# Kernel optimization log

Measured on AMD Instinct MI355X. Metric: run time of the kernel, lower is better.

Reference implementation:

```python
import jax, jax.numpy as jnp
import numpy as np

IN_DIM = 512
HID = 1024
E = 16
TOPK = 2


def setup_inputs() -> dict:
    key = jax.random.key(0)
    ks = jax.random.split(key, 8)
    s = 0.02
    x = jax.random.normal(ks[0], (4, 2048, IN_DIM), dtype=jnp.float32)
    Wr = jax.random.normal(ks[1], (IN_DIM, E), dtype=jnp.float32) * s
    br = jnp.zeros((E,), dtype=jnp.float32)
    W1 = jax.random.normal(ks[2], (E, IN_DIM, HID), dtype=jnp.float32) * s
    b1 = jnp.zeros((E, HID), dtype=jnp.float32)
    W2 = jax.random.normal(ks[3], (E, HID, IN_DIM), dtype=jnp.float32) * s
    b2 = jnp.zeros((E, IN_DIM), dtype=jnp.float32)
    return {"x": x, "Wr": Wr, "br": br, "W1": W1, "b1": b1, "W2": W2, "b2": b2}


def reference(x, Wr, br, W1, b1, W2, b2):
    token_shape = x.shape[:-1]
    xf = x.reshape(-1, x.shape[-1])            # [T, D]
    T = xf.shape[0]

    # router (temperature = 1.0)
    logits = xf @ Wr + br                       # [T, E]
    probs = jax.nn.softmax(logits, axis=-1)
    topk_w, topk_idx = jax.lax.top_k(probs, TOPK)           # [T, K]
    topk_w = topk_w / jnp.maximum(topk_w.sum(-1, keepdims=True), 1e-9)

    # combine weights: [T, E], zero where not routed
    combine = jnp.zeros((T, E), dtype=xf.dtype).at[
        jnp.arange(T)[:, None], topk_idx].add(topk_w)

    # per-expert MLP (exact GELU, as torch nn.GELU default), weighted combine
    y = jnp.zeros_like(xf)
    for e in range(E):
        h = jax.nn.gelu(xf @ W1[e] + b1[e], approximate=False)  # [T, H]
        o = h @ W2[e] + b2[e]                                   # [T, D]
        y = y + combine[:, e:e + 1] * o

    # residual (in_dim == out_dim)
    y = xf + y
    return y.reshape(*token_shape, IN_DIM)
```

## Files before the change

### kernel.cpp

```cpp
#include <hip/hip_runtime.h>
#include <hip/hip_bf16.h>
#include <math.h>

#define IN_DIM 512
#define HID    1024
#define NE     16
#define T_TOK  8192
#define NPAIR  (T_TOK*2)

typedef __attribute__((ext_vector_type(8))) short bf16x8;
typedef __attribute__((ext_vector_type(8))) unsigned short ushort8;
typedef __attribute__((ext_vector_type(4))) float f32x4;

__device__ __forceinline__ unsigned short f2b(float f){
  unsigned u = __float_as_uint(f);
  u += 0x7FFF + ((u >> 16) & 1);
  return (unsigned short)(u >> 16);
}
__device__ __forceinline__ float b2f(unsigned short u){
  return __uint_as_float(((unsigned)u) << 16);
}

__device__ __forceinline__ void barrier_lds_only(){
  asm volatile("s_waitcnt lgkmcnt(0)" ::: "memory");
  __builtin_amdgcn_s_barrier();
}

__global__ __launch_bounds__(256) void fused_head(
    const float* __restrict__ x, const float* __restrict__ Wr, const float* __restrict__ br,
    unsigned short* __restrict__ xb, int* __restrict__ eid, float* __restrict__ pw,
    const float* __restrict__ W1, unsigned short* __restrict__ O1,
    const float* __restrict__ W2, unsigned short* __restrict__ O2)
{
  __shared__ float tile[64][65];
  const int b = blockIdx.x;
  const int tid = threadIdx.x;

  if (b < 2048){
    int wid = tid >> 6, lane = tid & 63;
    int t = b*4 + wid;
    const float4* xr4 = (const float4*)(x + (size_t)t*IN_DIM);
    ushort4*      xb4 = (ushort4*)(xb + (size_t)t*IN_DIM);

    float acc[NE];
    #pragma unroll
    for (int i=0;i<NE;i++) acc[i]=0.f;

    #pragma unroll
    for (int j=0;j<2;j++){
      int f = j*64 + lane;
      float4 v = xr4[f];
      ushort4 o; o.x=f2b(v.x); o.y=f2b(v.y); o.z=f2b(v.z); o.w=f2b(v.w);
      xb4[f] = o;
      const float4* wr4 = (const float4*)(Wr + (size_t)(f*4)*NE);
      const float* vv = (const float*)&v;
      #pragma unroll
      for (int rr=0; rr<4; rr++){
        float xv = vv[rr];
        #pragma unroll
        for (int q=0;q<4;q++){
          float4 w = wr4[rr*4+q];
          acc[q*4+0] += xv*w.x; acc[q*4+1] += xv*w.y;
          acc[q*4+2] += xv*w.z; acc[q*4+3] += xv*w.w;
        }
      }
    }
    #pragma unroll
    for (int off=32; off>=1; off>>=1){
      #pragma unroll
      for (int i=0;i<NE;i++) acc[i] += __shfl_xor(acc[i], off, 64);
    }
    if (lane==0){
      #pragma unroll
      for (int i=0;i<NE;i++) acc[i] += br[i];
      int e0=0; float l0=acc[0];
      #pragma unroll
      for (int i=1;i<NE;i++) if (acc[i] > l0){ l0=acc[i]; e0=i; }
      int e1=-1; float l1=-3.0e38f;
      #pragma unroll
      for (int i=0;i<NE;i++) if (i!=e0 && acc[i] > l1){ l1=acc[i]; e1=i; }
      float w0 = 1.f/(1.f + __expf(l1 - l0));
      float w1 = 1.f - w0;
      pw[t*2+0] = w0; pw[t*2+1] = w1;
      eid[t*2+0] = e0; eid[t*2+1] = e1;
    }
    return;
  }

  const float* src; unsigned short* dst; int M, N, m0, n0;
  if (b < 4096){
    int b1 = b - 2048; M = IN_DIM; N = HID;
    int e = b1 >> 7, r = b1 & 127;
    n0 = (r & 15)*64; m0 = (r >> 4)*64;
    src = W1 + (size_t)e*M*N; dst = O1 + (size_t)e*M*N;
  } else {
    int b2 = b - 4096; M = HID; N = IN_DIM;
    int e = b2 >> 7, r = b2 & 127;
    n0 = (r & 7)*64; m0 = (r >> 3)*64;
    src = W2 + (size_t)e*M*N; dst = O2 + (size_t)e*M*N;
  }
  const int lr = tid >> 4, lc = (tid & 15)*4;
  #pragma unroll
  for (int i=0;i<4;i++)
    *(float4*)&tile[lr + i*16][lc] = *(const float4*)&src[(size_t)(m0 + lr + i*16)*N + n0 + lc];
  __syncthreads();
  const int nr = tid >> 3, mc = (tid & 7)*8;
  #pragma unroll
  for (int p=0;p<2;p++){
    int n = nr + p*32;
    ushort8 o;
    #pragma unroll
    for (int j=0;j<8;j++) o[j] = f2b(tile[mc+j][n]);
    *(ushort8*)&dst[(size_t)(n0 + n)*M + m0 + mc] = o;
  }
}

__global__ __launch_bounds__(1024) void bucket_kernel(const int* __restrict__ eid,
                                                      int* __restrict__ cnt,
                                                      int* __restrict__ bucket){
  int e = blockIdx.x;
  __shared__ int lbase;
  if (threadIdx.x == 0) lbase = 0;
  __syncthreads();
  int lane = threadIdx.x & 63, wid = threadIdx.x >> 6;
  int* be = bucket + e*T_TOK;
  for (int c = wid*64; c < NPAIR; c += 1024){
    int p = c + lane;
    bool ok = (eid[p] == e);
    unsigned long long m = __ballot(ok);
    int rank = __popcll(m & ((1ull << lane) - 1ull));
    int count = __popcll(m);
    int base = 0;
    if (lane == 0) base = atomicAdd(&lbase, count);
    base = __shfl(base, 0, 64);
    if (ok) be[base + rank] = p;
  }
  __syncthreads();
  if (threadIdx.x == 0) cnt[e] = lbase;
}

template<int KDIM, int NDIM, bool FIRST>
__global__ __launch_bounds__(256) void moe_gemm(
    const unsigned short* __restrict__ A,
    const unsigned short* __restrict__ Bm,
    const float* __restrict__ bias,
    const int* __restrict__ cnt,
    const int* __restrict__ bucket,
    const float* __restrict__ pw,
    unsigned short* __restrict__ hb,
    unsigned short* __restrict__ opb)
{
  constexpr int NS  = KDIM / 32;
  constexpr int NBT = NDIM / 128;

  int ntiles = 0;
  #pragma unroll
  for (int j=0;j<NE;j++) ntiles += ((cnt[j]+63)>>6)*NBT;

  __shared__ unsigned short As[2*64*32];
  __shared__ unsigned short Bs[2*128*32];

  int tid = threadIdx.x;
  int lane = tid & 63, wid = tid >> 6;
  int wm = (wid>>1)*32, wn = (wid&1)*64;
  int lr0 = tid >> 2;
  int c   = tid & 3;
  int sc  = (c ^ ((lr0 >> 1) & 3)) * 8;
  int wA  = lr0*32 + sc;
  int fr = lane & 15, fb = lane >> 4;
  int pf8 = (fb ^ ((fr >> 1) & 3)) * 8;
  int fq = (lane>>4)*4;

  const int t0 = (blockIdx.x & 7)*(gridDim.x >> 3) + (blockIdx.x >> 3);
  for (int t = t0; t < ntiles; t += gridDim.x){
    int e=0, tloc=0, ebase=0, ce=0, itl=1;
    {
      int cum=0, crow=0;
      #pragma unroll
      for (int j=0;j<NE;j++){
        int cj = cnt[j];
        int it = (cj+63)>>6;
        int tj = it * NBT;
        bool in = (t >= cum) & (t < cum+tj);
        if (in){ e=j; tloc=t-cum; ebase=crow; ce=cj; itl=it; }
        cum += tj; crow += cj;
      }
    }
    int i0 = (tloc % itl) * 64;
    int n0 = (tloc / itl) * 128;

    const int* buck = bucket + e*T_TOK;
    int posA = i0 + lr0;
    int arow;
    if (FIRST){
      int pair = (posA < ce) ? buck[posA] : buck[i0];
      arow = pair >> 1;
    } else {
      arow = ebase + posA;
      if (arow > NPAIR-1) arow = NPAIR-1;
    }
    const unsigned short* Ag = A + (size_t)arow*KDIM + c*8;
    const unsigned short* Bg = Bm + (size_t)e*NDIM*KDIM + (size_t)(n0 + lr0)*KDIM + c*8;

    f32x4 acc[2][4];
    #pragma unroll
    for (int a=0;a<2;a++)
      #pragma unroll
      for (int b=0;b<4;b++)
        #pragma unroll
        for (int j=0;j<4;j++) acc[a][b][j] = 0.f;

    float4 ar, br0, br1;
    ar  = *(const float4*)(Ag);
    br0 = *(const float4*)(Bg);
    br1 = *(const float4*)(Bg + (size_t)64*KDIM);
    *(float4*)(As + wA) = ar;
    *(float4*)(Bs + wA) = br0;
    *(float4*)(Bs + wA + 64*32) = br1;
    ar  = *(const float4*)(Ag + 32);
    br0 = *(const float4*)(Bg + 32);
    br1 = *(const float4*)(Bg + (size_t)64*KDIM + 32);
    barrier_lds_only();

    #pragma unroll 2
    for (int k = 0; k < NS; k++){
      const int cur = k & 1, nxt = cur ^ 1;
      float4 na, nb0, nb1;
      bool ld = (k + 2 < NS);
      if (ld){
        na  = *(const float4*)(Ag + (k+2)*32);
        nb0 = *(const float4*)(Bg + (k+2)*32);
        nb1 = *(const float4*)(Bg + (size_t)64*KDIM + (k+2)*32);
      }
      if (k + 1 < NS){
        *(float4*)(As + nxt*2048 + wA) = ar;
        *(float4*)(Bs + nxt*4096 + wA) = br0;
        *(float4*)(Bs + nxt*4096 + wA + 64*32) = br1;
      }
      if (ld){ ar = na; br0 = nb0; br1 = nb1; }

      const unsigned short* Ac = As + cur*2048;
      const unsigned short* Bc = Bs + cur*4096;
      bf16x8 af[2], bfr[4];
      #pragma unroll
      for (int s=0;s<2;s++) af[s]  = *(const bf16x8*)(Ac + (wm + s*16 + fr)*32 + pf8);
      #pragma unroll
      for (int u=0;u<4;u++) bfr[u] = *(const bf16x8*)(Bc + (wn + u*16 + fr)*32 + pf8);
      #pragma unroll
      for (int s=0;s<2;s++)
        #pragma unroll
        for (int u=0;u<4;u++)
          acc[s][u] = __builtin_amdgcn_mfma_f32_16x16x32_bf16(af[s], bfr[u], acc[s][u], 0,0,0);
      barrier_lds_only();
    }

    #pragma unroll
    for (int s=0;s<2;s++){
      #pragma unroll
      for (int i=0;i<4;i++){
        int row = wm + s*16 + fq + i;
        int pos = i0 + row;
        if (pos >= ce) continue;
        #pragma unroll
        for (int u=0;u<4;u++){
          int n = n0 + wn + u*16 + fr;
          float v = acc[s][u][i] + bias[e*NDIM + n];
          if (FIRST){
            float z2 = v*(1.5957691216057308f + 0.0713548162726009f*v*v);
            float g  = __fdividef(v, 1.f + __expf(-z2));
            hb[(size_t)(ebase + pos)*NDIM + n] = f2b(g);
          } else {
            int pair = buck[pos];
            opb[(size_t)pair*NDIM + n] = f2b(pw[pair]*v);
          }
        }
      }
    }
  }
}

__global__ __launch_bounds__(256) void combine_kernel(const float* __restrict__ x,
                                                      const unsigned short* __restrict__ opb,
                                                      float* __restrict__ out){
  int i = blockIdx.x*256 + threadIdx.x;
  int t  = i >> 7;
  int c4 = i & 127;
  float4 v = ((const float4*)x)[i];
  ushort4 a = ((const ushort4*)opb)[(size_t)(2*t)*128 + c4];
  ushort4 b = ((const ushort4*)opb)[(size_t)(2*t+1)*128 + c4];
  v.x += b2f(a.x) + b2f(b.x);
  v.y += b2f(a.y) + b2f(b.y);
  v.z += b2f(a.z) + b2f(b.z);
  v.w += b2f(a.w) + b2f(b.w);
  ((float4*)out)[i] = v;
}

extern "C" void kernel_launch(void* const* d_in, const int* in_sizes, int n_in,
                              void* d_out, int out_size, void* d_ws, size_t ws_size,
                              hipStream_t stream)
{
  const float* x  = (const float*)d_in[0];
  const float* Wr = (const float*)d_in[1];
  const float* br = (const float*)d_in[2];
  const float* W1 = (const float*)d_in[3];
  const float* b1 = (const float*)d_in[4];
  const float* W2 = (const float*)d_in[5];
  const float* b2 = (const float*)d_in[6];
  float* out = (float*)d_out;
  char* ws = (char*)d_ws;

  int*            cnt    = (int*)(ws + 0);
  int*            bucket = (int*)(ws + 1024);
  float*          pw     = (float*)(ws + 525312);
  unsigned short* xb     = (unsigned short*)(ws + 590848);
  unsigned short* w1t    = (unsigned short*)(ws + 8979456);
  unsigned short* w2t    = (unsigned short*)(ws + 25756672);
  unsigned short* hb     = (unsigned short*)(ws + 42533888);
  int*            eid    = (int*)(ws + 42533888);
  unsigned short* opb    = w1t;

  fused_head<<<6144, 256, 0, stream>>>(x, Wr, br, xb, eid, pw, W1, w1t, W2, w2t);
  bucket_kernel<<<NE, 1024, 0, stream>>>(eid, cnt, bucket);
  moe_gemm<IN_DIM, HID, true ><<<1024, 256, 0, stream>>>(
      xb, w1t, b1, cnt, bucket, pw, hb, opb);
  moe_gemm<HID, IN_DIM, false><<<1024, 256, 0, stream>>>(
      hb, w2t, b2, cnt, bucket, pw, hb, opb);
  combine_kernel<<<(T_TOK*IN_DIM/4)/256, 256, 0, stream>>>(x, opb, out);
}
```

Before: 250.0 us.

## Restructure router into 64 blocks of 128 tokens with LDS-staged x

The router part of the fused head kernel now has 64 blocks, each handling 128 tokens, instead of 2048 blocks of one token per wavefront. It stages x chunks in swizzled shared memory and has one thread per token accumulate all 16 logits, which removes the 64-lane shuffle reduction and the repeated Wr loads per token. The trade-off is much less parallelism for the router work: only 128 threads per block compute, with a sequential loop over 8 chunks. This relies on overlapping that work with the weight-transpose blocks launched in the same grid.

Result: slower. 272.2 us (+8.9%).

```diff
diff --git a/kernel.cpp b/kernel.cpp
--- a/kernel.cpp
+++ b/kernel.cpp
@@ -7,6 +7,7 @@
 #define NE     16
 #define T_TOK  8192
 #define NPAIR  (T_TOK*2)
+#define NRB    64
 
 typedef __attribute__((ext_vector_type(8))) short bf16x8;
 typedef __attribute__((ext_vector_type(8))) unsigned short ushort8;
@@ -32,47 +33,49 @@
     const float* __restrict__ W1, unsigned short* __restrict__ O1,
     const float* __restrict__ W2, unsigned short* __restrict__ O2)
 {
-  __shared__ float tile[64][65];
+  __shared__ __align__(16) char smraw[32768];
   const int b = blockIdx.x;
-  const int tid = threadIdx.x;
-
-  if (b < 2048){
-    int wid = tid >> 6, lane = tid & 63;
-    int t = b*4 + wid;
-    const float4* xr4 = (const float4*)(x + (size_t)t*IN_DIM);
-    ushort4*      xb4 = (ushort4*)(xb + (size_t)t*IN_DIM);
-
+  const int t = threadIdx.x;
+
+  if (b < NRB){
+    float (*xs)[64] = (float(*)[64])smraw;
+    const int T0 = b*128;
+    const int tq = t & 15, ts = t >> 4;
     float acc[NE];
     #pragma unroll
-    for (int i=0;i<NE;i++) acc[i]=0.f;
-
-    #pragma unroll
-    for (int j=0;j<2;j++){
-      int f = j*64 + lane;
-      float4 v = xr4[f];
-      ushort4 o; o.x=f2b(v.x); o.y=f2b(v.y); o.z=f2b(v.z); o.w=f2b(v.w);
-      xb4[f] = o;
-      const float4* wr4 = (const float4*)(Wr + (size_t)(f*4)*NE);
-      const float* vv = (const float*)&v;
-      #pragma unroll
-      for (int rr=0; rr<4; rr++){
-        float xv = vv[rr];
+    for (int e=0;e<NE;e++) acc[e] = 0.f;
+    const bool comp = (t < 128);
+
+    #pragma unroll 1
+    for (int c = 0; c < 8; ++c){
+      #pragma unroll
+      for (int s = 0; s < 8; ++s){
+        int tok = s*16 + ts;
+        const float4 v = *(const float4*)&x[(size_t)(T0+tok)*IN_DIM + c*64 + tq*4];
+        ushort4 o; o.x=f2b(v.x); o.y=f2b(v.y); o.z=f2b(v.z); o.w=f2b(v.w);
+        *(ushort4*)&xb[(size_t)(T0+tok)*IN_DIM + c*64 + tq*4] = o;
+        *(float4*)&xs[tok][(tq ^ (tok & 15))*4] = v;
+      }
+      __syncthreads();
+      if (comp){
         #pragma unroll
-        for (int q=0;q<4;q++){
-          float4 w = wr4[rr*4+q];
-          acc[q*4+0] += xv*w.x; acc[q*4+1] += xv*w.y;
-          acc[q*4+2] += xv*w.z; acc[q*4+3] += xv*w.w;
+        for (int cc = 0; cc < 16; ++cc){
+          const float4 xv = *(const float4*)&xs[t][(cc ^ (t & 15))*4];
+          const float* wr = &Wr[(size_t)(c*64 + cc*4)*NE];
+          #pragma unroll
+          for (int j=0;j<4;j++){
+            const float xvj = ((const float*)&xv)[j];
+            #pragma unroll
+            for (int e=0;e<NE;e++) acc[e] += xvj * wr[j*NE + e];
+          }
         }
       }
-    }
-    #pragma unroll
-    for (int off=32; off>=1; off>>=1){
-      #pragma unroll
-      for (int i=0;i<NE;i++) acc[i] += __shfl_xor(acc[i], off, 64);
-    }
-    if (lane==0){
-      #pragma unroll
-      for (int i=0;i<NE;i++) acc[i] += br[i];
+      __syncthreads();
+    }
+
+    if (comp){
+      #pragma unroll
+      for (int e=0;e<NE;e++) acc[e] += br[e];
       int e0=0; float l0=acc[0];
       #pragma unroll
       for (int i=1;i<NE;i++) if (acc[i] > l0){ l0=acc[i]; e0=i; }
@@ -81,30 +84,33 @@
       for (int i=0;i<NE;i++) if (i!=e0 && acc[i] > l1){ l1=acc[i]; e1=i; }
       float w0 = 1.f/(1.f + __expf(l1 - l0));
       float w1 = 1.f - w0;
-      pw[t*2+0] = w0; pw[t*2+1] = w1;
-      eid[t*2+0] = e0; eid[t*2+1] = e1;
+      int tok = T0 + t;
+      pw[tok*2+0] = w0; pw[tok*2+1] = w1;
+      eid[tok*2+0] = e0; eid[tok*2+1] = e1;
     }
     return;
   }
 
+  float (*tile)[65] = (float(*)[65])smraw;
   const float* src; unsigned short* dst; int M, N, m0, n0;
-  if (b < 4096){
-    int b1 = b - 2048; M = IN_DIM; N = HID;
-    int e = b1 >> 7, r = b1 & 127;
+  const int bb = b - NRB;
+  if (bb < 2048){
+    M = IN_DIM; N = HID;
+    int e = bb >> 7, r = bb & 127;
     n0 = (r & 15)*64; m0 = (r >> 4)*64;
     src = W1 + (size_t)e*M*N; dst = O1 + (size_t)e*M*N;
   } else {
-    int b2 = b - 4096; M = HID; N = IN_DIM;
+    int b2 = bb - 2048; M = HID; N = IN_DIM;
     int e = b2 >> 7, r = b2 & 127;
     n0 = (r & 7)*64; m0 = (r >> 3)*64;
     src = W2 + (size_t)e*M*N; dst = O2 + (size_t)e*M*N;
   }
-  const int lr = tid >> 4, lc = (tid & 15)*4;
+  const int lr = t >> 4, lc = (t & 15)*4;
   #pragma unroll
   for (int i=0;i<4;i++)
     *(float4*)&tile[lr + i*16][lc] = *(const float4*)&src[(size_t)(m0 + lr + i*16)*N + n0 + lc];
   __syncthreads();
-  const int nr = tid >> 3, mc = (tid & 7)*8;
+  const int nr = t >> 3, mc = (t & 7)*8;
   #pragma unroll
   for (int p=0;p<2;p++){
     int n = nr + p*32;
@@ -206,9 +212,9 @@
     #pragma unroll
     for (int a=0;a<2;a++)
       #pragma unroll
-      for (int b=0;b<4;b++)
+      for (int b2=0;b2<4;b2++)
         #pragma unroll
-        for (int j=0;j<4;j++) acc[a][b][j] = 0.f;
+        for (int j=0;j<4;j++) acc[a][b2][j] = 0.f;
 
     float4 ar, br0, br1;
     ar  = *(const float4*)(Ag);
@@ -319,7 +325,7 @@
   int*            eid    = (int*)(ws + 42533888);
   unsigned short* opb    = w1t;
 
-  fused_head<<<6144, 256, 0, stream>>>(x, Wr, br, xb, eid, pw, W1, w1t, W2, w2t);
+  fused_head<<<NRB + 4096, 256, 0, stream>>>(x, Wr, br, xb, eid, pw, W1, w1t, W2, w2t);
   bucket_kernel<<<NE, 1024, 0, stream>>>(eid, cnt, bucket);
   moe_gemm<IN_DIM, HID, true ><<<1024, 256, 0, stream>>>(
       xb, w1t, b1, cnt, bucket, pw, hb, opb);
```

## Fuse expert bucketing into router via global atomics, drop bucket kernel

Applied to the files above, without the earlier changes.

The router lanes now reserve slots in per-expert buckets with global atomicAdd on counters cleared by a memset, which removes the separate bucket_kernel launch and the eid intermediate. The first expert GEMM's grid also grows from 1024 to 2048 blocks. Bucket order becomes nondeterministic, and contended atomics on 16 counters from 8192 tokens may serialize. There is also an extra memset launch.

New measurement: 401.5 us. 1.61x slower.

```diff
diff --git a/kernel.cpp b/kernel.cpp
--- a/kernel.cpp
+++ b/kernel.cpp
@@ -28,7 +28,8 @@
 
 __global__ __launch_bounds__(256) void fused_head(
     const float* __restrict__ x, const float* __restrict__ Wr, const float* __restrict__ br,
-    unsigned short* __restrict__ xb, int* __restrict__ eid, float* __restrict__ pw,
+    unsigned short* __restrict__ xb, int* __restrict__ cnt, int* __restrict__ bucket,
+    float* __restrict__ pw,
     const float* __restrict__ W1, unsigned short* __restrict__ O1,
     const float* __restrict__ W2, unsigned short* __restrict__ O2)
 {
@@ -82,19 +83,23 @@
       float w0 = 1.f/(1.f + __expf(l1 - l0));
       float w1 = 1.f - w0;
       pw[t*2+0] = w0; pw[t*2+1] = w1;
-      eid[t*2+0] = e0; eid[t*2+1] = e1;
+      int s0 = atomicAdd(&cnt[e0], 1);
+      bucket[e0*T_TOK + s0] = t*2+0;
+      int s1 = atomicAdd(&cnt[e1], 1);
+      bucket[e1*T_TOK + s1] = t*2+1;
     }
     return;
   }
 
   const float* src; unsigned short* dst; int M, N, m0, n0;
-  if (b < 4096){
-    int b1 = b - 2048; M = IN_DIM; N = HID;
-    int e = b1 >> 7, r = b1 & 127;
+  const int bb = b - 2048;
+  if (bb < 2048){
+    M = IN_DIM; N = HID;
+    int e = bb >> 7, r = bb & 127;
     n0 = (r & 15)*64; m0 = (r >> 4)*64;
     src = W1 + (size_t)e*M*N; dst = O1 + (size_t)e*M*N;
   } else {
-    int b2 = b - 4096; M = HID; N = IN_DIM;
+    int b2 = bb - 2048; M = HID; N = IN_DIM;
     int e = b2 >> 7, r = b2 & 127;
     n0 = (r & 7)*64; m0 = (r >> 3)*64;
     src = W2 + (size_t)e*M*N; dst = O2 + (size_t)e*M*N;
@@ -115,30 +120,6 @@
   }
 }
 
-__global__ __launch_bounds__(1024) void bucket_kernel(const int* __restrict__ eid,
-                                                      int* __restrict__ cnt,
-                                                      int* __restrict__ bucket){
-  int e = blockIdx.x;
-  __shared__ int lbase;
-  if (threadIdx.x == 0) lbase = 0;
-  __syncthreads();
-  int lane = threadIdx.x & 63, wid = threadIdx.x >> 6;
-  int* be = bucket + e*T_TOK;
-  for (int c = wid*64; c < NPAIR; c += 1024){
-    int p = c + lane;
-    bool ok = (eid[p] == e);
-    unsigned long long m = __ballot(ok);
-    int rank = __popcll(m & ((1ull << lane) - 1ull));
-    int count = __popcll(m);
-    int base = 0;
-    if (lane == 0) base = atomicAdd(&lbase, count);
-    base = __shfl(base, 0, 64);
-    if (ok) be[base + rank] = p;
-  }
-  __syncthreads();
-  if (threadIdx.x == 0) cnt[e] = lbase;
-}
-
 template<int KDIM, int NDIM, bool FIRST>
 __global__ __launch_bounds__(256) void moe_gemm(
     const unsigned short* __restrict__ A,
@@ -206,9 +187,9 @@
     #pragma unroll
     for (int a=0;a<2;a++)
       #pragma unroll
-      for (int b=0;b<4;b++)
+      for (int b2=0;b2<4;b2++)
         #pragma unroll
-        for (int j=0;j<4;j++) acc[a][b][j] = 0.f;
+        for (int j=0;j<4;j++) acc[a][b2][j] = 0.f;
 
     float4 ar, br0, br1;
     ar  = *(const float4*)(Ag);
@@ -316,12 +297,12 @@
   unsigned short* w1t    = (unsigned short*)(ws + 8979456);
   unsigned short* w2t    = (unsigned short*)(ws + 25756672);
   unsigned short* hb     = (unsigned short*)(ws + 42533888);
-  int*            eid    = (int*)(ws + 42533888);
   unsigned short* opb    = w1t;
 
-  fused_head<<<6144, 256, 0, stream>>>(x, Wr, br, xb, eid, pw, W1, w1t, W2, w2t);
-  bucket_kernel<<<NE, 1024, 0, stream>>>(eid, cnt, bucket);
-  moe_gemm<IN_DIM, HID, true ><<<1024, 256, 0, stream>>>(
+  hipMemsetAsync(cnt, 0, NE*sizeof(int), stream);
+
+  fused_head<<<6144, 256, 0, stream>>>(x, Wr, br, xb, cnt, bucket, pw, W1, w1t, W2, w2t);
+  moe_gemm<IN_DIM, HID, true ><<<2048, 256, 0, stream>>>(
       xb, w1t, b1, cnt, bucket, pw, hb, opb);
   moe_gemm<HID, IN_DIM, false><<<1024, 256, 0, stream>>>(
       hb, w2t, b2, cnt, bucket, pw, hb, opb);
```
